# Kernel optimization log

Measured on AMD Instinct MI355X. Metric: run time of the kernel, lower is better.

The kernel has to match this reference:

```python
import jax, jax.numpy as jnp
import numpy as np

D = 256; NH = 8; NL = 4; NP = 4; HD = D // NH
LEVELS = ((80, 80), (40, 40), (20, 20), (10, 10))
B = 8; LTXT = 32
LVIS = sum(h * w for h, w in LEVELS)  # 8500


def layer_norm(x, g, b):
    m = x.mean(-1, keepdims=True)
    v = ((x - m) ** 2).mean(-1, keepdims=True)
    return (x - m) * jax.lax.rsqrt(v + 1e-5) * g + b


def gelu(x):
    return jax.nn.gelu(x, approximate=False)


def sample_level(v, H, W, loc):
    # v: [B,NH,H*W,HD] level value; loc: [B,Lq,NH,NP,2] normalized [0,1] (x,y)
    # bilinear, align_corners=False, zero padding (matches grid_sample in MSDeformAttn)
    x = loc[..., 0] * W - 0.5
    y = loc[..., 1] * H - 0.5
    x0 = jnp.floor(x); y0 = jnp.floor(y)
    fx = x - x0; fy = y - y0
    Bq, Lq = loc.shape[0], loc.shape[1]
    out = jnp.zeros((Bq, NH, Lq * NP, HD), v.dtype)
    for dx in (0, 1):
        for dy in (0, 1):
            xi = x0 + dx; yi = y0 + dy
            w = (fx if dx else 1.0 - fx) * (fy if dy else 1.0 - fy)
            valid = (xi >= 0) & (xi < W) & (yi >= 0) & (yi < H)
            xi_c = jnp.clip(xi, 0, W - 1).astype(jnp.int32)
            yi_c = jnp.clip(yi, 0, H - 1).astype(jnp.int32)
            idx = (yi_c * W + xi_c).transpose(0, 2, 1, 3).reshape(Bq, NH, Lq * NP)
            wv = jnp.where(valid, w, 0.0).transpose(0, 2, 1, 3).reshape(Bq, NH, Lq * NP, 1)
            g = jnp.take_along_axis(v, idx[..., None], axis=2)  # [B,NH,Lq*NP,HD]
            out = out + g * wv
    return out.reshape(Bq, NH, Lq, NP, HD)


def setup_inputs() -> dict:
    key = jax.random.key(0)
    ks = iter(jax.random.split(key, 64))
    def rn(shape, s=1.0):
        return jax.random.normal(next(ks), shape, jnp.float32) * s
    inp = {}
    inp['txt_tokens'] = rn((B, LTXT, D))
    inp['vis_tokens'] = rn((B, LVIS, D))
    for i, (H, W) in enumerate(LEVELS):
        inp[f'feat{i}'] = rn((B, D, H, W))
    inp['spatial_shapes'] = jnp.array(LEVELS, jnp.int32)
    starts = np.cumsum([0] + [h * w for h, w in LEVELS])[:NL]
    inp['level_start_index'] = jnp.array(starts, jnp.int32)
    inp['reference_points'] = jax.random.uniform(next(ks), (B, LTXT, NL, 2), jnp.float32)
    inp['txt_pos'] = rn((B, LTXT, D), 0.02)
    inp['vis_pos'] = rn((B, LVIS, D), 0.02)
    s = 0.02
    # MSDeformAttn params
    inp['W_off'] = rn((D, NH * NL * NP * 2), s); inp['b_off'] = rn((NH * NL * NP * 2,), s)
    inp['W_aw'] = rn((D, NH * NL * NP), s); inp['b_aw'] = rn((NH * NL * NP,), s)
    inp['W_v'] = rn((D, D), s); inp['b_v'] = rn((D,), s)
    inp['W_do'] = rn((D, D), s); inp['b_do'] = rn((D,), s)
    # adapter projections
    inp['W_q_lvi'] = rn((D, D), s); inp['b_q_lvi'] = rn((D,), s)
    inp['W_out_lvi'] = rn((D, D), s); inp['b_out_lvi'] = rn((D,), s)
    # lvi norms + ffn
    inp['ln1_g'] = jnp.ones((D,)); inp['ln1_b'] = jnp.zeros((D,))
    inp['ln2_g'] = jnp.ones((D,)); inp['ln2_b'] = jnp.zeros((D,))
    inp['ffn1_W1'] = rn((D, 4 * D), s); inp['ffn1_b1'] = rn((4 * D,), s)
    inp['ffn1_W2'] = rn((4 * D, D), s); inp['ffn1_b2'] = rn((D,), s)
    # vli MultiheadAttention
    inp['Wq_m'] = rn((D, D), s); inp['bq_m'] = rn((D,), s)
    inp['Wk_m'] = rn((D, D), s); inp['bk_m'] = rn((D,), s)
    inp['Wv_m'] = rn((D, D), s); inp['bv_m'] = rn((D,), s)
    inp['Wo_m'] = rn((D, D), s); inp['bo_m'] = rn((D,), s)
    inp['vln1_g'] = jnp.ones((D,)); inp['vln1_b'] = jnp.zeros((D,))
    inp['vln2_g'] = jnp.ones((D,)); inp['vln2_b'] = jnp.zeros((D,))
    inp['ffn2_W1'] = rn((D, 4 * D), s); inp['ffn2_b1'] = rn((4 * D,), s)
    inp['ffn2_W2'] = rn((4 * D, D), s); inp['ffn2_b2'] = rn((D,), s)
    return inp


def reference(txt_tokens, vis_tokens, feat0, feat1, feat2, feat3, reference_points, txt_pos, vis_pos,
              W_off, b_off, W_aw, b_aw, W_v, b_v, W_do, b_do,
              W_q_lvi, b_q_lvi, W_out_lvi, b_out_lvi,
              ln1_g, ln1_b, ln2_g, ln2_b,
              ffn1_W1, ffn1_b1, ffn1_W2, ffn1_b2,
              Wq_m, bq_m, Wk_m, bk_m, Wv_m, bv_m, Wo_m, bo_m,
              vln1_g, vln1_b, vln2_g, vln2_b,
              ffn2_W1, ffn2_b1, ffn2_W2, ffn2_b2,
              spatial_shapes, level_start_index):
    # ---- lvi: deformable multi-scale attention (txt queries sample vis features) ----
    txt_query = txt_tokens + txt_pos
    q = txt_query @ W_q_lvi + b_q_lvi
    feats = (feat0, feat1, feat2, feat3)
    value = jnp.concatenate([f.reshape(f.shape[0], D, -1).transpose(0, 2, 1) for f in feats], axis=1)
    v = (value @ W_v + b_v).reshape(B, LVIS, NH, HD)
    off = (q @ W_off + b_off).reshape(B, LTXT, NH, NL, NP, 2)
    aw = jax.nn.softmax((q @ W_aw + b_aw).reshape(B, LTXT, NH, NL * NP), axis=-1).reshape(B, LTXT, NH, NL, NP)
    normalizer = jnp.array([[w, h] for h, w in LEVELS], jnp.float32)  # (W,H) per level
    loc = reference_points[:, :, None, :, None, :] + off / normalizer[None, None, None, :, None, :]
    acc = jnp.zeros((B, NH, LTXT, HD), v.dtype)
    start = 0
    for l, (H, W) in enumerate(LEVELS):
        vl = v[:, start:start + H * W].transpose(0, 2, 1, 3)  # [B,NH,HW,HD]
        s = sample_level(vl, H, W, loc[:, :, :, l])           # [B,NH,Lq,NP,HD]
        awl = aw[:, :, :, l].transpose(0, 2, 1, 3)[..., None]  # [B,NH,Lq,NP,1]
        acc = acc + (s * awl).sum(3)
        start += H * W
    d_out = acc.transpose(0, 2, 1, 3).reshape(B, LTXT, D) @ W_do + b_do
    txt_attn = d_out @ W_out_lvi + b_out_lvi
    txt_res = layer_norm(txt_tokens + txt_attn, ln1_g, ln1_b)
    ff = gelu(txt_res @ ffn1_W1 + ffn1_b1) @ ffn1_W2 + ffn1_b2
    txt_res = layer_norm(txt_res + ff, ln2_g, ln2_b)
    # ---- vli: standard cross attention (vis queries attend txt) ----
    vis_query = vis_tokens + vis_pos
    vis_key = txt_res + txt_pos
    qh = (vis_query @ Wq_m + bq_m).reshape(B, LVIS, NH, HD)
    kh = (vis_key @ Wk_m + bk_m).reshape(B, LTXT, NH, HD)
    vh = (vis_key @ Wv_m + bv_m).reshape(B, LTXT, NH, HD)
    scores = jnp.einsum('bqhd,bkhd->bhqk', qh, kh) / np.float32(np.sqrt(HD))
    p = jax.nn.softmax(scores, axis=-1)
    mo = jnp.einsum('bhqk,bkhd->bqhd', p, vh).reshape(B, LVIS, D) @ Wo_m + bo_m
    vis_res = layer_norm(vis_tokens + mo, vln1_g, vln1_b)
    ff2 = gelu(vis_res @ ffn2_W1 + ffn2_b1) @ ffn2_W2 + ffn2_b2
    vis_res = layer_norm(vis_res + ff2, vln2_g, vln2_b)
    attn_weights = p.mean(axis=1)  # torch MHA averages over heads
    return (txt_res, vis_res, attn_weights)
```

## Files before the change

kernel.cpp:

```cpp
#include <hip/hip_runtime.h>
#include <cstddef>

#define DD   256
#define NHH  8
#define HDD  32
#define BB   8
#define LT   32
#define LV   8500

typedef unsigned short u16;
typedef unsigned int   u32;
typedef __attribute__((ext_vector_type(8))) short short8;
typedef __attribute__((ext_vector_type(8))) unsigned short ushort8;
typedef __attribute__((ext_vector_type(4))) float f32x4;

__device__ __forceinline__ float gelu_f(float x) {
  return 0.5f * x * (1.0f + erff(x * 0.70710678118654752440f));
}

__device__ __forceinline__ u16 f2bf(float x) {
  u32 u = __float_as_uint(x);
  u += 0x7FFFu + ((u >> 16) & 1u);
  return (u16)(u >> 16);
}
__device__ __forceinline__ float bf2f(u16 h) { return __uint_as_float((u32)h << 16); }

enum { AM_PLAIN = 0, AM_ADD = 1, AM_FEAT = 2 };
enum { EP_BIAS = 0, EP_GELU = 1, EP_ACC = 2 };

template<int BM, int BN, int TM, int TN, int AMODE, int EPI>
__launch_bounds__(256)
__global__ void gemm_k(const float* __restrict__ A0, const float* __restrict__ A1,
                       const float* __restrict__ Wt, const float* __restrict__ bias,
                       float* __restrict__ C, int M, int K, int ldw, int ldc)
{
  constexpr int BK = 16;
  __shared__ __align__(16) float As[BK][BM];
  __shared__ __align__(16) float Ws[BK][BN];
  const int tid  = threadIdx.x;
  const int row0 = blockIdx.x * BM;
  const int col0 = blockIdx.y * BN;
  const int tx = tid % (BN / TN);
  const int ty = tid / (BN / TN);
  float acc[TM][TN] = {};

  for (int k0 = 0; k0 < K; k0 += BK) {
    {
      constexpr int AU = BM * BK / 4;
      for (int u = tid; u < AU; u += 256) {
        int m  = u / (BK / 4);
        int kq = (u % (BK / 4)) * 4;
        int grow = row0 + m;
        float4 v = make_float4(0.f, 0.f, 0.f, 0.f);
        if (grow < M) {
          v = *(const float4*)(A0 + (size_t)grow * K + k0 + kq);
          if constexpr (AMODE == AM_ADD) {
            float4 w = *(const float4*)(A1 + (size_t)grow * K + k0 + kq);
            v.x += w.x; v.y += w.y; v.z += w.z; v.w += w.w;
          }
        }
        As[kq + 0][m] = v.x; As[kq + 1][m] = v.y;
        As[kq + 2][m] = v.z; As[kq + 3][m] = v.w;
      }
    }
    {
      constexpr int WU = BK * BN / 4;
      for (int u = tid; u < WU; u += 256) {
        int k  = u / (BN / 4);
        int n4 = (u % (BN / 4)) * 4;
        *(float4*)&Ws[k][n4] =
            *(const float4*)(Wt + (size_t)(k0 + k) * ldw + col0 + n4);
      }
    }
    __syncthreads();

    #pragma unroll
    for (int k = 0; k < BK; ++k) {
      float a[TM], bv[TN];
      #pragma unroll
      for (int i = 0; i < TM; ++i) a[i] = As[k][ty * TM + i];
      #pragma unroll
      for (int j = 0; j < TN; j += 4) {
        float4 t4 = *(const float4*)&Ws[k][tx * TN + j];
        bv[j] = t4.x; bv[j + 1] = t4.y; bv[j + 2] = t4.z; bv[j + 3] = t4.w;
      }
      #pragma unroll
      for (int i = 0; i < TM; ++i)
        #pragma unroll
        for (int j = 0; j < TN; ++j)
          acc[i][j] = fmaf(a[i], bv[j], acc[i][j]);
    }
    __syncthreads();
  }

  #pragma unroll
  for (int i = 0; i < TM; ++i) {
    int r = row0 + ty * TM + i;
    if (r >= M) continue;
    #pragma unroll
    for (int j4 = 0; j4 < TN; j4 += 4) {
      int c = col0 + tx * TN + j4;
      float4 v = make_float4(acc[i][j4], acc[i][j4 + 1], acc[i][j4 + 2], acc[i][j4 + 3]);
      float4 b4 = *(const float4*)(bias + c);
      v.x += b4.x; v.y += b4.y; v.z += b4.z; v.w += b4.w;
      if constexpr (EPI == EP_GELU) {
        v.x = gelu_f(v.x); v.y = gelu_f(v.y); v.z = gelu_f(v.z); v.w = gelu_f(v.w);
      }
      *(float4*)(C + (size_t)r * ldc + c) = v;
    }
  }
}

__global__ void wsplit_kernel(const float* __restrict__ W, u16* __restrict__ hi,
                              u16* __restrict__ lo, int total, int Nw)
{
  int id = blockIdx.x * 256 + threadIdx.x;
  if (id >= total) return;
  int k = id / Nw, n = id - k * Nw;
  float x = W[id];
  u16 h = f2bf(x);
  u16 l = f2bf(x - bf2f(h));
  int o = ((k >> 3) * Nw + n) * 8 + (k & 7);
  hi[o] = h; lo[o] = l;
}

template<int AMODE, int EPI>
__global__ __launch_bounds__(256) void mgemm(
    const void* __restrict__ Ap, const float* __restrict__ A1,
    const u16* __restrict__ Whi, const u16* __restrict__ Wlo,
    const float* __restrict__ bias, void* __restrict__ Cp,
    int M, int K, int lda, int ldc, int Nw, int wcol0, int ks0,
    const float* __restrict__ f0, const float* __restrict__ f1,
    const float* __restrict__ f2, const float* __restrict__ f3)
{
  __shared__ __align__(16) u16 Ahi[4 * 129 * 8];
  __shared__ __align__(16) u16 Alo[4 * 129 * 8];
  const int tid  = threadIdx.x;
  const int lane = tid & 63;
  const int w    = tid >> 6;
  const int wr   = w >> 1, wc = w & 1;
  const int row0  = blockIdx.x * 128;
  const int colC0 = blockIdx.y * 128;
  f32x4 acc[4][4] = {};

  const int nk = K >> 5;
  for (int kt = 0; kt < nk; ++kt) {
    if constexpr (AMODE == 3) {
      const u16* Ab = (const u16*)Ap;
      #pragma unroll
      for (int p = 0; p < 2; ++p) {
        int j = tid + p * 256;
        int row = j >> 2, slot = j & 3;
        int gr = row0 + row;
        ushort8 v = {};
        if (gr < M) v = *(const ushort8*)(Ab + (size_t)gr * lda + kt * 32 + slot * 8);
        *(ushort8*)&Ahi[(slot * 129 + row) * 8] = v;
      }
    } else {
      #pragma unroll
      for (int p = 0; p < 4; ++p) {
        int j = tid + p * 256;
        int row, f4;
        if constexpr (AMODE == 2) { f4 = j >> 7; row = j & 127; }
        else                      { row = j >> 3; f4 = j & 7; }
        int gr = row0 + row;
        float4 v = make_float4(0.f, 0.f, 0.f, 0.f);
        if (gr < M) {
          if constexpr (AMODE == 2) {
            int b = gr / LV;
            int s = gr - b * LV;
            int l = (s >= 8400) ? 3 : (s >= 8000) ? 2 : (s >= 6400) ? 1 : 0;
            const float* fp = (l == 0) ? f0 : (l == 1) ? f1 : (l == 2) ? f2 : f3;
            const int hw = (l == 0) ? 6400 : (l == 1) ? 1600 : (l == 2) ? 400 : 100;
            const int st = (l == 0) ? 0 : (l == 1) ? 6400 : (l == 2) ? 8000 : 8400;
            const float* base = fp + ((size_t)b * DD + (kt * 32 + f4 * 4)) * hw + (s - st);
            v.x = base[0];
            v.y = base[(size_t)hw];
            v.z = base[2 * (size_t)hw];
            v.w = base[3 * (size_t)hw];
          } else {
            const float* Af = (const float*)Ap;
            v = *(const float4*)(Af + (size_t)gr * lda + kt * 32 + f4 * 4);
            if constexpr (AMODE == 1) {
              float4 u2 = *(const float4*)(A1 + (size_t)gr * lda + kt * 32 + f4 * 4);
              v.x += u2.x; v.y += u2.y; v.z += u2.z; v.w += u2.w;
            }
          }
        }
        int slot = f4 >> 1, half = f4 & 1;
        int off = (slot * 129 + row) * 8 + half * 4;
        u16 h0 = f2bf(v.x), h1 = f2bf(v.y), h2 = f2bf(v.z), h3 = f2bf(v.w);
        uint2 hp; hp.x = (u32)h0 | ((u32)h1 << 16); hp.y = (u32)h2 | ((u32)h3 << 16);
        *(uint2*)&Ahi[off] = hp;
        u16 l0 = f2bf(v.x - bf2f(h0)), l1 = f2bf(v.y - bf2f(h1));
        u16 l2 = f2bf(v.z - bf2f(h2)), l3 = f2bf(v.w - bf2f(h3));
        uint2 lp; lp.x = (u32)l0 | ((u32)l1 << 16); lp.y = (u32)l2 | ((u32)l3 << 16);
        *(uint2*)&Alo[off] = lp;
      }
    }
    __syncthreads();

    const int slot = lane >> 4;
    const int lrow = lane & 15;
    short8 ah[4], al[4], bh[4], bl[4];
    #pragma unroll
    for (int m = 0; m < 4; ++m) {
      int off = (slot * 129 + wr * 64 + m * 16 + lrow) * 8;
      ah[m] = *(const short8*)&Ahi[off];
      if constexpr (AMODE != 3) al[m] = *(const short8*)&Alo[off];
    }
    #pragma unroll
    for (int n = 0; n < 4; ++n) {
      size_t off = ((size_t)((ks0 + kt) * 4 + slot) * Nw + wcol0 + colC0 + wc * 64 + n * 16 + lrow) * 8;
      bh[n] = *(const short8*)(Whi + off);
      bl[n] = *(const short8*)(Wlo + off);
    }
    #pragma unroll
    for (int m = 0; m < 4; ++m)
      #pragma unroll
      for (int n = 0; n < 4; ++n) {
        acc[m][n] = __builtin_amdgcn_mfma_f32_16x16x32_bf16(ah[m], bh[n], acc[m][n], 0, 0, 0);
        acc[m][n] = __builtin_amdgcn_mfma_f32_16x16x32_bf16(ah[m], bl[n], acc[m][n], 0, 0, 0);
        if constexpr (AMODE != 3)
          acc[m][n] = __builtin_amdgcn_mfma_f32_16x16x32_bf16(al[m], bh[n], acc[m][n], 0, 0, 0);
      }
    __syncthreads();
  }

  const int lrow = lane & 15;
  #pragma unroll
  for (int m = 0; m < 4; ++m) {
    #pragma unroll
    for (int j = 0; j < 4; ++j) {
      int r = row0 + wr * 64 + m * 16 + ((lane >> 4) << 2) + j;
      if (r >= M) continue;
      #pragma unroll
      for (int n = 0; n < 4; ++n) {
        int c = colC0 + wc * 64 + n * 16 + lrow;
        float v = acc[m][n][j];
        if constexpr (EPI == 0) {
          ((float*)Cp)[(size_t)r * ldc + c] = v + bias[c];
        } else if constexpr (EPI == 1) {
          ((u16*)Cp)[(size_t)r * ldc + c] = f2bf(gelu_f(v + bias[c]));
        } else {
          ((float*)Cp)[(size_t)r * ldc + c] += v;
        }
      }
    }
  }
}

__global__ void ln_kernel(const float* __restrict__ X, const float* __restrict__ R,
                          const float* __restrict__ g, const float* __restrict__ bta,
                          float* __restrict__ O, int M)
{
  int row  = blockIdx.x * 4 + (threadIdx.x >> 6);
  int lane = threadIdx.x & 63;
  if (row >= M) return;
  size_t base = (size_t)row * DD + lane * 4;
  float4 x = *(const float4*)(X + base);
  float4 r = *(const float4*)(R + base);
  x.x += r.x; x.y += r.y; x.z += r.z; x.w += r.w;
  float s  = x.x + x.y + x.z + x.w;
  float s2 = x.x * x.x + x.y * x.y + x.z * x.z + x.w * x.w;
  #pragma unroll
  for (int m = 1; m < 64; m <<= 1) {
    s  += __shfl_xor(s, m);
    s2 += __shfl_xor(s2, m);
  }
  float mean = s * (1.0f / 256.0f);
  float var  = s2 * (1.0f / 256.0f) - mean * mean;
  float rstd = rsqrtf(var + 1e-5f);
  float4 gg = *(const float4*)(g + lane * 4);
  float4 bb = *(const float4*)(bta + lane * 4);
  float4 o;
  o.x = (x.x - mean) * rstd * gg.x + bb.x;
  o.y = (x.y - mean) * rstd * gg.y + bb.y;
  o.z = (x.z - mean) * rstd * gg.z + bb.z;
  o.w = (x.w - mean) * rstd * gg.w + bb.w;
  *(float4*)(O + base) = o;
}

__global__ void softloc_kernel(const float* __restrict__ awl, const float* __restrict__ offb,
                               const float* __restrict__ refp, float* __restrict__ aw,
                               float* __restrict__ loc)
{
  int idx = blockIdx.x * 256 + threadIdx.x;
  if (idx >= BB * LT * NHH) return;
  int h   = idx & 7;
  int row = idx >> 3;
  float v[16]; float mx = -1e30f;
  #pragma unroll
  for (int i = 0; i < 16; ++i) { v[i] = awl[row * 128 + h * 16 + i]; mx = fmaxf(mx, v[i]); }
  float sum = 0.f;
  #pragma unroll
  for (int i = 0; i < 16; ++i) { v[i] = expf(v[i] - mx); sum += v[i]; }
  float inv = 1.0f / sum;
  #pragma unroll
  for (int i = 0; i < 16; ++i) aw[row * 128 + h * 16 + i] = v[i] * inv;
  const float invn[4] = {1.f / 80.f, 1.f / 40.f, 1.f / 20.f, 1.f / 10.f};
  #pragma unroll
  for (int l = 0; l < 4; ++l) {
    float rx = refp[(row * 4 + l) * 2 + 0];
    float ry = refp[(row * 4 + l) * 2 + 1];
    #pragma unroll
    for (int p = 0; p < 4; ++p) {
      int o = row * 256 + h * 32 + l * 8 + p * 2;
      loc[o + 0] = rx + offb[o + 0] * invn[l];
      loc[o + 1] = ry + offb[o + 1] * invn[l];
    }
  }
}

__global__ void sampler_kernel(const float* __restrict__ vproj, const float* __restrict__ loc,
                               const float* __restrict__ aw, float* __restrict__ acc)
{
  int row = blockIdx.x;
  int t   = threadIdx.x;
  int h   = t >> 5, hd = t & 31;
  int b   = row >> 5;
  const float* vb = vproj + (size_t)b * LV * DD;
  const int Hs[4] = {80, 40, 20, 10};
  const int st[4] = {0, 6400, 8000, 8400};
  float a = 0.f;
  #pragma unroll
  for (int l = 0; l < 4; ++l) {
    const int Wl = Hs[l], Hl = Hs[l];
    #pragma unroll
    for (int p = 0; p < 4; ++p) {
      int o = row * 256 + h * 32 + l * 8 + p * 2;
      float lx  = loc[o + 0];
      float ly  = loc[o + 1];
      float wgt = aw[row * 128 + h * 16 + l * 4 + p];
      float x = lx * (float)Wl - 0.5f;
      float y = ly * (float)Hl - 0.5f;
      float x0f = floorf(x), y0f = floorf(y);
      float fx = x - x0f, fy = y - y0f;
      int x0 = (int)x0f, y0 = (int)y0f;
      #pragma unroll
      for (int dy = 0; dy < 2; ++dy) {
        #pragma unroll
        for (int dx = 0; dx < 2; ++dx) {
          int xi = x0 + dx, yi = y0 + dy;
          float w2 = (dx ? fx : 1.f - fx) * (dy ? fy : 1.f - fy);
          if (xi >= 0 && xi < Wl && yi >= 0 && yi < Hl) {
            a = fmaf(wgt * w2, vb[(size_t)(st[l] + yi * Wl + xi) * DD + h * 32 + hd], a);
          }
        }
      }
    }
  }
  acc[(size_t)row * DD + t] = a;
}

__global__ __launch_bounds__(512)
void attn_kernel(const float* __restrict__ qh, const float* __restrict__ kh,
                 const float* __restrict__ vh, float* __restrict__ mo,
                 float* __restrict__ awout)
{
  __shared__ __align__(16) float Ks[32][256];
  __shared__ __align__(16) float Vs[32][256];
  const int b = blockIdx.y;
  {
    const float4* ksrc = (const float4*)(kh + (size_t)b * 32 * DD);
    const float4* vsrc = (const float4*)(vh + (size_t)b * 32 * DD);
    float4* kd = (float4*)&Ks[0][0];
    float4* vd = (float4*)&Vs[0][0];
    for (int u = threadIdx.x; u < 2048; u += 512) { kd[u] = ksrc[u]; vd[u] = vsrc[u]; }
  }
  __syncthreads();

  const int rl   = threadIdx.x >> 5;
  const int l    = threadIdx.x & 31;
  const int h    = l >> 2;
  const int part = l & 3;
  const int s    = blockIdx.x * 16 + rl;
  if (s >= LV) return;
  const size_t row = (size_t)b * LV + s;
  const int c0 = h * 32 + part * 8;
  const float scale = 0.17677669529663687f;

  float q[8];
  {
    const float4* qp = (const float4*)(qh + row * DD + c0);
    float4 a = qp[0], c = qp[1];
    q[0]=a.x; q[1]=a.y; q[2]=a.z; q[3]=a.w; q[4]=c.x; q[5]=c.y; q[6]=c.z; q[7]=c.w;
  }

  float sc[32]; float mx = -1e30f;
  #pragma unroll
  for (int k = 0; k < 32; ++k) {
    const float4* kp = (const float4*)&Ks[k][c0];
    float4 a = kp[0], c = kp[1];
    float d = 0.f;
    d = fmaf(q[0], a.x, d); d = fmaf(q[1], a.y, d); d = fmaf(q[2], a.z, d); d = fmaf(q[3], a.w, d);
    d = fmaf(q[4], c.x, d); d = fmaf(q[5], c.y, d); d = fmaf(q[6], c.z, d); d = fmaf(q[7], c.w, d);
    d += __shfl_xor(d, 1);
    d += __shfl_xor(d, 2);
    sc[k] = d * scale;
    mx = fmaxf(mx, sc[k]);
  }
  float sum = 0.f;
  #pragma unroll
  for (int k = 0; k < 32; ++k) { sc[k] = expf(sc[k] - mx); sum += sc[k]; }
  const float inv = 1.0f / sum;
  #pragma unroll
  for (int k = 0; k < 32; ++k) sc[k] *= inv;

  float o[8] = {};
  #pragma unroll
  for (int k = 0; k < 32; ++k) {
    const float4* vp = (const float4*)&Vs[k][c0];
    float4 a = vp[0], c = vp[1];
    const float pk = sc[k];
    o[0] = fmaf(pk, a.x, o[0]); o[1] = fmaf(pk, a.y, o[1]);
    o[2] = fmaf(pk, a.z, o[2]); o[3] = fmaf(pk, a.w, o[3]);
    o[4] = fmaf(pk, c.x, o[4]); o[5] = fmaf(pk, c.y, o[5]);
    o[6] = fmaf(pk, c.z, o[6]); o[7] = fmaf(pk, c.w, o[7]);
  }
  {
    float4* op = (float4*)(mo + row * DD + c0);
    op[0] = make_float4(o[0], o[1], o[2], o[3]);
    op[1] = make_float4(o[4], o[5], o[6], o[7]);
  }
  #pragma unroll
  for (int k = 0; k < 32; ++k) {
    float v = sc[k];
    v += __shfl_xor(v, 4);
    v += __shfl_xor(v, 8);
    v += __shfl_xor(v, 16);
    if (h == 0 && (k >> 3) == part) awout[row * 32 + k] = v * 0.125f;
  }
}

extern "C" void kernel_launch(void* const* d_in, const int* in_sizes, int n_in,
                              void* d_out, int out_size, void* d_ws, size_t ws_size,
                              hipStream_t stream)
{
  const float* txt_tokens = (const float*)d_in[0];
  const float* vis_tokens = (const float*)d_in[1];
  const float* feat0 = (const float*)d_in[2];
  const float* feat1 = (const float*)d_in[3];
  const float* feat2 = (const float*)d_in[4];
  const float* feat3 = (const float*)d_in[5];
  const float* refp    = (const float*)d_in[8];
  const float* txt_pos = (const float*)d_in[9];
  const float* vis_pos = (const float*)d_in[10];
  const float* W_off = (const float*)d_in[11]; const float* b_off = (const float*)d_in[12];
  const float* W_aw  = (const float*)d_in[13]; const float* b_aw  = (const float*)d_in[14];
  const float* W_v   = (const float*)d_in[15]; const float* b_v   = (const float*)d_in[16];
  const float* W_do  = (const float*)d_in[17]; const float* b_do  = (const float*)d_in[18];
  const float* W_q   = (const float*)d_in[19]; const float* b_q   = (const float*)d_in[20];
  const float* W_out = (const float*)d_in[21]; const float* b_out = (const float*)d_in[22];
  const float* ln1_g = (const float*)d_in[23]; const float* ln1_b = (const float*)d_in[24];
  const float* ln2_g = (const float*)d_in[25]; const float* ln2_b = (const float*)d_in[26];
  const float* f1W1  = (const float*)d_in[27]; const float* f1b1  = (const float*)d_in[28];
  const float* f1W2  = (const float*)d_in[29]; const float* f1b2  = (const float*)d_in[30];
  const float* Wq_m  = (const float*)d_in[31]; const float* bq_m  = (const float*)d_in[32];
  const float* Wk_m  = (const float*)d_in[33]; const float* bk_m  = (const float*)d_in[34];
  const float* Wv_m  = (const float*)d_in[35]; const float* bv_m  = (const float*)d_in[36];
  const float* Wo_m  = (const float*)d_in[37]; const float* bo_m  = (const float*)d_in[38];
  const float* vln1_g = (const float*)d_in[39]; const float* vln1_b = (const float*)d_in[40];
  const float* vln2_g = (const float*)d_in[41]; const float* vln2_b = (const float*)d_in[42];
  const float* f2W1  = (const float*)d_in[43]; const float* f2b1  = (const float*)d_in[44];
  const float* f2W2  = (const float*)d_in[45]; const float* f2b2  = (const float*)d_in[46];

  const int MV = BB * LV;
  float* ws = (float*)d_ws;
  const size_t BIG = (size_t)MV * DD;
  float* buf0 = ws;
  float* buf1 = ws + BIG;
  float* buf2 = ws + 2 * BIG;
  float* sm   = ws + 3 * BIG;
  float* qb    = sm;
  float* offb  = qb + 65536;
  float* awlb  = offb + 65536;
  float* awb   = awlb + 32768;
  float* locb  = awb + 32768;
  float* accb  = locb + 65536;
  float* doutb = accb + 65536;
  float* tattn = doutb + 65536;
  float* tres1 = tattn + 65536;
  float* ffh   = tres1 + 65536;
  float* ffb   = ffh + 262144;
  float* khb   = ffb + 65536;
  float* vhb   = khb + 65536;
  u16* wsp   = (u16*)(vhb + 65536);
  u16* wv_hi = wsp;               u16* wv_lo = wv_hi + 65536;
  u16* wq_hi = wv_lo + 65536;     u16* wq_lo = wq_hi + 65536;
  u16* wo_hi = wq_lo + 65536;     u16* wo_lo = wo_hi + 65536;
  u16* w1_hi = wo_lo + 65536;     u16* w1_lo = w1_hi + 262144;
  u16* w2_hi = w1_lo + 262144;    u16* w2_lo = w2_hi + 262144;

  float* out_txt = (float*)d_out;
  float* out_vis = out_txt + (size_t)BB * LT * DD;
  float* out_aw  = out_vis + BIG;

  dim3 blk(256);
  #define NOF nullptr, nullptr, nullptr, nullptr

  wsplit_kernel<<<256, blk, 0, stream>>>(W_v,  wv_hi, wv_lo, 65536, 256);
  wsplit_kernel<<<256, blk, 0, stream>>>(Wq_m, wq_hi, wq_lo, 65536, 256);
  wsplit_kernel<<<256, blk, 0, stream>>>(Wo_m, wo_hi, wo_lo, 65536, 256);
  wsplit_kernel<<<1024, blk, 0, stream>>>(f2W1, w1_hi, w1_lo, 262144, 1024);
  wsplit_kernel<<<1024, blk, 0, stream>>>(f2W2, w2_hi, w2_lo, 262144, 256);

  mgemm<2, 0><<<dim3(532, 2), blk, 0, stream>>>(
      nullptr, nullptr, wv_hi, wv_lo, b_v, buf0, MV, DD, DD, DD, DD, 0, 0,
      feat0, feat1, feat2, feat3);
  mgemm<1, 0><<<dim3(532, 2), blk, 0, stream>>>(
      vis_tokens, vis_pos, wq_hi, wq_lo, bq_m, buf1, MV, DD, DD, DD, DD, 0, 0, NOF);

  gemm_k<32,64,2,4,AM_ADD,EP_BIAS><<<dim3(8,4), blk, 0, stream>>>(
      txt_tokens, txt_pos, W_q, b_q, qb, 256, DD, DD, DD);
  gemm_k<32,64,2,4,AM_PLAIN,EP_BIAS><<<dim3(8,4), blk, 0, stream>>>(
      qb, nullptr, W_off, b_off, offb, 256, DD, DD, DD);
  gemm_k<32,64,2,4,AM_PLAIN,EP_BIAS><<<dim3(8,2), blk, 0, stream>>>(
      qb, nullptr, W_aw, b_aw, awlb, 256, DD, 128, 128);
  softloc_kernel<<<8, blk, 0, stream>>>(awlb, offb, refp, awb, locb);
  sampler_kernel<<<256, blk, 0, stream>>>(buf0, locb, awb, accb);
  gemm_k<32,64,2,4,AM_PLAIN,EP_BIAS><<<dim3(8,4), blk, 0, stream>>>(
      accb, nullptr, W_do, b_do, doutb, 256, DD, DD, DD);
  gemm_k<32,64,2,4,AM_PLAIN,EP_BIAS><<<dim3(8,4), blk, 0, stream>>>(
      doutb, nullptr, W_out, b_out, tattn, 256, DD, DD, DD);
  ln_kernel<<<64, blk, 0, stream>>>(tattn, txt_tokens, ln1_g, ln1_b, tres1, 256);
  gemm_k<32,64,2,4,AM_PLAIN,EP_GELU><<<dim3(8,16), blk, 0, stream>>>(
      tres1, nullptr, f1W1, f1b1, ffh, 256, DD, 1024, 1024);
  gemm_k<32,64,2,4,AM_PLAIN,EP_BIAS><<<dim3(8,4), blk, 0, stream>>>(
      ffh, nullptr, f1W2, f1b2, ffb, 256, 1024, DD, DD);
  ln_kernel<<<64, blk, 0, stream>>>(ffb, tres1, ln2_g, ln2_b, out_txt, 256);

  gemm_k<32,64,2,4,AM_ADD,EP_BIAS><<<dim3(8,4), blk, 0, stream>>>(
      out_txt, txt_pos, Wk_m, bk_m, khb, 256, DD, DD, DD);
  gemm_k<32,64,2,4,AM_ADD,EP_BIAS><<<dim3(8,4), blk, 0, stream>>>(
      out_txt, txt_pos, Wv_m, bv_m, vhb, 256, DD, DD, DD);

  attn_kernel<<<dim3(532, 8), dim3(512), 0, stream>>>(buf1, khb, vhb, buf2, out_aw);
  mgemm<0, 0><<<dim3(532, 2), blk, 0, stream>>>(
      buf2, nullptr, wo_hi, wo_lo, bo_m, buf0, MV, DD, DD, DD, DD, 0, 0, NOF);
  ln_kernel<<<17000, blk, 0, stream>>>(buf0, vis_tokens, vln1_g, vln1_b, buf1, MV);

  for (int c = 0; c < 2; ++c) {
    mgemm<0, 1><<<dim3(532, 4), blk, 0, stream>>>(
        buf1, nullptr, w1_hi, w1_lo, f2b1 + c * 512, buf2,
        MV, DD, DD, 512, 1024, c * 512, 0, NOF);
    if (c == 0) {
      mgemm<3, 0><<<dim3(532, 2), blk, 0, stream>>>(
          buf2, nullptr, w2_hi, w2_lo, f2b2, buf0,
          MV, 512, 512, DD, DD, 0, 0, NOF);
    } else {
      mgemm<3, 2><<<dim3(532, 2), blk, 0, stream>>>(
          buf2, nullptr, w2_hi, w2_lo, nullptr, buf0,
          MV, 512, 512, DD, DD, 0, 16, NOF);
    }
  }
  ln_kernel<<<17000, blk, 0, stream>>>(buf0, buf1, vln2_g, vln2_b, out_vis, MV);
  #undef NOF
}
```

Baseline: 1.302 ms.

## Pre-split activations to bf16 hi/lo and double-buffer A tiles via global_load_lds

The attention kernel and the first vision LayerNorm now write their outputs already split into bf16 hi/lo pairs. The matching GEMMs can then stream A tiles straight into LDS with global_load_lds, double-buffered, instead of converting fp32 in registers on every tile. The attention kernel also stops staging K/V in shared memory and reads them from global/cache directly. The second LayerNorm rebuilds the residual from the hi/lo pair, which changes the intermediate precision slightly. Overall this trades extra activation write traffic for removing per-tile conversion work and overlapping loads with MFMA.

```diff
diff --git a/kernel.cpp b/kernel.cpp
--- a/kernel.cpp
+++ b/kernel.cpp
@@ -25,7 +25,13 @@
 }
 __device__ __forceinline__ float bf2f(u16 h) { return __uint_as_float((u32)h << 16); }
 
-enum { AM_PLAIN = 0, AM_ADD = 1, AM_FEAT = 2 };
+__device__ __forceinline__ void gload16(const u16* g, u16* l) {
+  __builtin_amdgcn_global_load_lds(
+      (const __attribute__((address_space(1))) void*)g,
+      (__attribute__((address_space(3))) void*)l, 16, 0, 0);
+}
+
+enum { AM_PLAIN = 0, AM_ADD = 1, AM_FEAT = 2, AM_HI = 3, AM_SPLIT = 4 };
 enum { EP_BIAS = 0, EP_GELU = 1, EP_ACC = 2 };
 
 template<int BM, int BN, int TM, int TN, int AMODE, int EPI>
@@ -126,15 +132,16 @@
 
 template<int AMODE, int EPI>
 __global__ __launch_bounds__(256) void mgemm(
-    const void* __restrict__ Ap, const float* __restrict__ A1,
+    const void* __restrict__ Ap, const void* __restrict__ A1p,
     const u16* __restrict__ Whi, const u16* __restrict__ Wlo,
     const float* __restrict__ bias, void* __restrict__ Cp,
     int M, int K, int lda, int ldc, int Nw, int wcol0, int ks0,
     const float* __restrict__ f0, const float* __restrict__ f1,
     const float* __restrict__ f2, const float* __restrict__ f3)
 {
-  __shared__ __align__(16) u16 Ahi[4 * 129 * 8];
-  __shared__ __align__(16) u16 Alo[4 * 129 * 8];
+  constexpr bool GL = (AMODE >= 3);
+  constexpr int SMEM_U16 = GL ? (AMODE == AM_SPLIT ? 16384 : 8192) : 8256;
+  __shared__ __align__(16) u16 smem[SMEM_U16];
   const int tid  = threadIdx.x;
   const int lane = tid & 63;
   const int w    = tid >> 6;
@@ -142,31 +149,68 @@
   const int row0  = blockIdx.x * 128;
   const int colC0 = blockIdx.y * 128;
   f32x4 acc[4][4] = {};
-
   const int nk = K >> 5;
-  for (int kt = 0; kt < nk; ++kt) {
-    if constexpr (AMODE == 3) {
-      const u16* Ab = (const u16*)Ap;
+
+  if constexpr (GL) {
+    const u16* Ah = (const u16*)Ap;
+    const u16* Al = (const u16*)A1p;
+    auto stage = [&](int t, int buf) {
       #pragma unroll
       for (int p = 0; p < 2; ++p) {
-        int j = tid + p * 256;
-        int row = j >> 2, slot = j & 3;
-        int gr = row0 + row;
-        ushort8 v = {};
-        if (gr < M) v = *(const ushort8*)(Ab + (size_t)gr * lda + kt * 32 + slot * 8);
-        *(ushort8*)&Ahi[(slot * 129 + row) * 8] = v;
-      }
-    } else {
+        int i = w + p * 4;
+        int r = row0 + i * 16 + (lane >> 2);
+        if (r >= M) r = M - 1;
+        size_t goff = (size_t)r * lda + t * 32 + (lane & 3) * 8;
+        gload16(Ah + goff, &smem[buf * 4096 + i * 512]);
+        if constexpr (AMODE == AM_SPLIT)
+          gload16(Al + goff, &smem[8192 + buf * 4096 + i * 512]);
+      }
+    };
+    stage(0, 0);
+    __syncthreads();
+    for (int kt = 0; kt < nk; ++kt) {
+      const int cur = kt & 1;
+      if (kt + 1 < nk) stage(kt + 1, cur ^ 1);
+      const int slot = lane >> 4;
+      const int lrow = lane & 15;
+      short8 ah[4], al[4], bh[4], bl[4];
+      #pragma unroll
+      for (int m = 0; m < 4; ++m) {
+        int off = cur * 4096 + (((wr * 64 + m * 16 + lrow) << 2) + slot) * 8;
+        ah[m] = *(const short8*)&smem[off];
+        if constexpr (AMODE == AM_SPLIT) al[m] = *(const short8*)&smem[8192 + off];
+      }
+      #pragma unroll
+      for (int n = 0; n < 4; ++n) {
+        size_t off = ((size_t)((ks0 + kt) * 4 + slot) * Nw + wcol0 + colC0 + wc * 64 + n * 16 + lrow) * 8;
+        bh[n] = *(const short8*)(Whi + off);
+        bl[n] = *(const short8*)(Wlo + off);
+      }
+      #pragma unroll
+      for (int m = 0; m < 4; ++m)
+        #pragma unroll
+        for (int n = 0; n < 4; ++n) {
+          acc[m][n] = __builtin_amdgcn_mfma_f32_16x16x32_bf16(ah[m], bh[n], acc[m][n], 0, 0, 0);
+          acc[m][n] = __builtin_amdgcn_mfma_f32_16x16x32_bf16(ah[m], bl[n], acc[m][n], 0, 0, 0);
+          if constexpr (AMODE == AM_SPLIT)
+            acc[m][n] = __builtin_amdgcn_mfma_f32_16x16x32_bf16(al[m], bh[n], acc[m][n], 0, 0, 0);
+        }
+      __syncthreads();
+    }
+  } else {
+    u16* Ahi = smem;
+    u16* Alo = smem + 4128;
+    for (int kt = 0; kt < nk; ++kt) {
       #pragma unroll
       for (int p = 0; p < 4; ++p) {
         int j = tid + p * 256;
         int row, f4;
-        if constexpr (AMODE == 2) { f4 = j >> 7; row = j & 127; }
-        else                      { row = j >> 3; f4 = j & 7; }
+        if constexpr (AMODE == AM_FEAT) { f4 = j >> 7; row = j & 127; }
+        else                            { row = j >> 3; f4 = j & 7; }
         int gr = row0 + row;
         float4 v = make_float4(0.f, 0.f, 0.f, 0.f);
         if (gr < M) {
-          if constexpr (AMODE == 2) {
+          if constexpr (AMODE == AM_FEAT) {
             int b = gr / LV;
             int s = gr - b * LV;
             int l = (s >= 8400) ? 3 : (s >= 8000) ? 2 : (s >= 6400) ? 1 : 0;
@@ -181,8 +225,8 @@
           } else {
             const float* Af = (const float*)Ap;
             v = *(const float4*)(Af + (size_t)gr * lda + kt * 32 + f4 * 4);
-            if constexpr (AMODE == 1) {
-              float4 u2 = *(const float4*)(A1 + (size_t)gr * lda + kt * 32 + f4 * 4);
+            if constexpr (AMODE == AM_ADD) {
+              float4 u2 = *(const float4*)((const float*)A1p + (size_t)gr * lda + kt * 32 + f4 * 4);
               v.x += u2.x; v.y += u2.y; v.z += u2.z; v.w += u2.w;
             }
           }
@@ -197,34 +241,33 @@
         uint2 lp; lp.x = (u32)l0 | ((u32)l1 << 16); lp.y = (u32)l2 | ((u32)l3 << 16);
         *(uint2*)&Alo[off] = lp;
       }
-    }
-    __syncthreads();
-
-    const int slot = lane >> 4;
-    const int lrow = lane & 15;
-    short8 ah[4], al[4], bh[4], bl[4];
-    #pragma unroll
-    for (int m = 0; m < 4; ++m) {
-      int off = (slot * 129 + wr * 64 + m * 16 + lrow) * 8;
-      ah[m] = *(const short8*)&Ahi[off];
-      if constexpr (AMODE != 3) al[m] = *(const short8*)&Alo[off];
-    }
-    #pragma unroll
-    for (int n = 0; n < 4; ++n) {
-      size_t off = ((size_t)((ks0 + kt) * 4 + slot) * Nw + wcol0 + colC0 + wc * 64 + n * 16 + lrow) * 8;
-      bh[n] = *(const short8*)(Whi + off);
-      bl[n] = *(const short8*)(Wlo + off);
-    }
-    #pragma unroll
-    for (int m = 0; m < 4; ++m)
+      __syncthreads();
+
+      const int slot = lane >> 4;
+      const int lrow = lane & 15;
+      short8 ah[4], al[4], bh[4], bl[4];
+      #pragma unroll
+      for (int m = 0; m < 4; ++m) {
+        int off = (slot * 129 + wr * 64 + m * 16 + lrow) * 8;
+        ah[m] = *(const short8*)&Ahi[off];
+        al[m] = *(const short8*)&Alo[off];
+      }
       #pragma unroll
       for (int n = 0; n < 4; ++n) {
-        acc[m][n] = __builtin_amdgcn_mfma_f32_16x16x32_bf16(ah[m], bh[n], acc[m][n], 0, 0, 0);
-        acc[m][n] = __builtin_amdgcn_mfma_f32_16x16x32_bf16(ah[m], bl[n], acc[m][n], 0, 0, 0);
-        if constexpr (AMODE != 3)
+        size_t off = ((size_t)((ks0 + kt) * 4 + slot) * Nw + wcol0 + colC0 + wc * 64 + n * 16 + lrow) * 8;
+        bh[n] = *(const short8*)(Whi + off);
+        bl[n] = *(const short8*)(Wlo + off);
+      }
+      #pragma unroll
+      for (int m = 0; m < 4; ++m)
+        #pragma unroll
+        for (int n = 0; n < 4; ++n) {
+          acc[m][n] = __builtin_amdgcn_mfma_f32_16x16x32_bf16(ah[m], bh[n], acc[m][n], 0, 0, 0);
+          acc[m][n] = __builtin_amdgcn_mfma_f32_16x16x32_bf16(ah[m], bl[n], acc[m][n], 0, 0, 0);
           acc[m][n] = __builtin_amdgcn_mfma_f32_16x16x32_bf16(al[m], bh[n], acc[m][n], 0, 0, 0);
-      }
-    __syncthreads();
+        }
+      __syncthreads();
+    }
   }
 
   const int lrow = lane & 15;
@@ -238,9 +281,9 @@
       for (int n = 0; n < 4; ++n) {
         int c = colC0 + wc * 64 + n * 16 + lrow;
         float v = acc[m][n][j];
-        if constexpr (EPI == 0) {
+        if constexpr (EPI == EP_BIAS) {
           ((float*)Cp)[(size_t)r * ldc + c] = v + bias[c];
-        } else if constexpr (EPI == 1) {
+        } else if constexpr (EPI == EP_GELU) {
           ((u16*)Cp)[(size_t)r * ldc + c] = f2bf(gelu_f(v + bias[c]));
         } else {
           ((float*)Cp)[(size_t)r * ldc + c] += v;
@@ -250,17 +293,7 @@
   }
 }
 
-__global__ void ln_kernel(const float* __restrict__ X, const float* __restrict__ R,
-                          const float* __restrict__ g, const float* __restrict__ bta,
-                          float* __restrict__ O, int M)
-{
-  int row  = blockIdx.x * 4 + (threadIdx.x >> 6);
-  int lane = threadIdx.x & 63;
-  if (row >= M) return;
-  size_t base = (size_t)row * DD + lane * 4;
-  float4 x = *(const float4*)(X + base);
-  float4 r = *(const float4*)(R + base);
-  x.x += r.x; x.y += r.y; x.z += r.z; x.w += r.w;
+__device__ __forceinline__ float4 ln_core(float4 x, const float* g, const float* bta, int lane) {
   float s  = x.x + x.y + x.z + x.w;
   float s2 = x.x * x.x + x.y * x.y + x.z * x.z + x.w * x.w;
   #pragma unroll
@@ -278,6 +311,61 @@
   o.y = (x.y - mean) * rstd * gg.y + bb.y;
   o.z = (x.z - mean) * rstd * gg.z + bb.z;
   o.w = (x.w - mean) * rstd * gg.w + bb.w;
+  return o;
+}
+
+__global__ void ln_kernel(const float* __restrict__ X, const float* __restrict__ R,
+                          const float* __restrict__ g, const float* __restrict__ bta,
+                          float* __restrict__ O, int M)
+{
+  int row  = blockIdx.x * 4 + (threadIdx.x >> 6);
+  int lane = threadIdx.x & 63;
+  if (row >= M) return;
+  size_t base = (size_t)row * DD + lane * 4;
+  float4 x = *(const float4*)(X + base);
+  float4 r = *(const float4*)(R + base);
+  x.x += r.x; x.y += r.y; x.z += r.z; x.w += r.w;
+  float4 o = ln_core(x, g, bta, lane);
+  *(float4*)(O + base) = o;
+}
+
+__global__ void ln_vis1(const float* __restrict__ X, const float* __restrict__ R,
+                        const float* __restrict__ g, const float* __restrict__ bta,
+                        u16* __restrict__ Oh, u16* __restrict__ Ol, int M)
+{
+  int row  = blockIdx.x * 4 + (threadIdx.x >> 6);
+  int lane = threadIdx.x & 63;
+  if (row >= M) return;
+  size_t base = (size_t)row * DD + lane * 4;
+  float4 x = *(const float4*)(X + base);
+  float4 r = *(const float4*)(R + base);
+  x.x += r.x; x.y += r.y; x.z += r.z; x.w += r.w;
+  float4 o = ln_core(x, g, bta, lane);
+  u16 h0 = f2bf(o.x), h1 = f2bf(o.y), h2 = f2bf(o.z), h3 = f2bf(o.w);
+  uint2 hp; hp.x = (u32)h0 | ((u32)h1 << 16); hp.y = (u32)h2 | ((u32)h3 << 16);
+  *(uint2*)(Oh + base) = hp;
+  u16 l0 = f2bf(o.x - bf2f(h0)), l1 = f2bf(o.y - bf2f(h1));
+  u16 l2 = f2bf(o.z - bf2f(h2)), l3 = f2bf(o.w - bf2f(h3));
+  uint2 lp; lp.x = (u32)l0 | ((u32)l1 << 16); lp.y = (u32)l2 | ((u32)l3 << 16);
+  *(uint2*)(Ol + base) = lp;
+}
+
+__global__ void ln_vis2(const float* __restrict__ X, const u16* __restrict__ Rh,
+                        const u16* __restrict__ Rl, const float* __restrict__ g,
+                        const float* __restrict__ bta, float* __restrict__ O, int M)
+{
+  int row  = blockIdx.x * 4 + (threadIdx.x >> 6);
+  int lane = threadIdx.x & 63;
+  if (row >= M) return;
+  size_t base = (size_t)row * DD + lane * 4;
+  float4 x = *(const float4*)(X + base);
+  uint2 hp = *(const uint2*)(Rh + base);
+  uint2 lp = *(const uint2*)(Rl + base);
+  x.x += bf2f((u16)hp.x) + bf2f((u16)lp.x);
+  x.y += bf2f((u16)(hp.x >> 16)) + bf2f((u16)(lp.x >> 16));
+  x.z += bf2f((u16)hp.y) + bf2f((u16)lp.y);
+  x.w += bf2f((u16)(hp.y >> 16)) + bf2f((u16)(lp.y >> 16));
+  float4 o = ln_core(x, g, bta, lane);
   *(float4*)(O + base) = o;
 }
 
@@ -355,30 +443,21 @@
 
 __global__ __launch_bounds__(512)
 void attn_kernel(const float* __restrict__ qh, const float* __restrict__ kh,
-                 const float* __restrict__ vh, float* __restrict__ mo,
-                 float* __restrict__ awout)
-{
-  __shared__ __align__(16) float Ks[32][256];
-  __shared__ __align__(16) float Vs[32][256];
-  const int b = blockIdx.y;
-  {
-    const float4* ksrc = (const float4*)(kh + (size_t)b * 32 * DD);
-    const float4* vsrc = (const float4*)(vh + (size_t)b * 32 * DD);
-    float4* kd = (float4*)&Ks[0][0];
-    float4* vd = (float4*)&Vs[0][0];
-    for (int u = threadIdx.x; u < 2048; u += 512) { kd[u] = ksrc[u]; vd[u] = vsrc[u]; }
-  }
-  __syncthreads();
-
-  const int rl   = threadIdx.x >> 5;
-  const int l    = threadIdx.x & 31;
-  const int h    = l >> 2;
+                 const float* __restrict__ vh, u16* __restrict__ mo_hi,
+                 u16* __restrict__ mo_lo, float* __restrict__ awout)
+{
+  const int b  = blockIdx.y;
+  const int rl = threadIdx.x >> 5;
+  const int l  = threadIdx.x & 31;
+  const int h  = l >> 2;
   const int part = l & 3;
-  const int s    = blockIdx.x * 16 + rl;
+  const int s  = blockIdx.x * 16 + rl;
   if (s >= LV) return;
   const size_t row = (size_t)b * LV + s;
   const int c0 = h * 32 + part * 8;
   const float scale = 0.17677669529663687f;
+  const float* Kb = kh + (size_t)b * 32 * DD;
+  const float* Vb = vh + (size_t)b * 32 * DD;
 
   float q[8];
   {
@@ -390,7 +469,7 @@
   float sc[32]; float mx = -1e30f;
   #pragma unroll
   for (int k = 0; k < 32; ++k) {
-    const float4* kp = (const float4*)&Ks[k][c0];
+    const float4* kp = (const float4*)(Kb + k * DD + c0);
     float4 a = kp[0], c = kp[1];
     float d = 0.f;
     d = fmaf(q[0], a.x, d); d = fmaf(q[1], a.y, d); d = fmaf(q[2], a.z, d); d = fmaf(q[3], a.w, d);
@@ -410,7 +489,7 @@
   float o[8] = {};
   #pragma unroll
   for (int k = 0; k < 32; ++k) {
-    const float4* vp = (const float4*)&Vs[k][c0];
+    const float4* vp = (const float4*)(Vb + k * DD + c0);
     float4 a = vp[0], c = vp[1];
     const float pk = sc[k];
     o[0] = fmaf(pk, a.x, o[0]); o[1] = fmaf(pk, a.y, o[1]);
@@ -419,9 +498,19 @@
     o[6] = fmaf(pk, c.z, o[6]); o[7] = fmaf(pk, c.w, o[7]);
   }
   {
-    float4* op = (float4*)(mo + row * DD + c0);
-    op[0] = make_float4(o[0], o[1], o[2], o[3]);
-    op[1] = make_float4(o[4], o[5], o[6], o[7]);
+    u16 hh[8], ll[8];
+    #pragma unroll
+    for (int j = 0; j < 8; ++j) {
+      hh[j] = f2bf(o[j]);
+      ll[j] = f2bf(o[j] - bf2f(hh[j]));
+    }
+    uint4 hp, lp;
+    hp.x = (u32)hh[0] | ((u32)hh[1] << 16); hp.y = (u32)hh[2] | ((u32)hh[3] << 16);
+    hp.z = (u32)hh[4] | ((u32)hh[5] << 16); hp.w = (u32)hh[6] | ((u32)hh[7] << 16);
+    lp.x = (u32)ll[0] | ((u32)ll[1] << 16); lp.y = (u32)ll[2] | ((u32)ll[3] << 16);
+    lp.z = (u32)ll[4] | ((u32)ll[5] << 16); lp.w = (u32)ll[6] | ((u32)ll[7] << 16);
+    *(uint4*)(mo_hi + row * DD + c0) = hp;
+    *(uint4*)(mo_lo + row * DD + c0) = lp;
   }
   #pragma unroll
   for (int k = 0; k < 32; ++k) {
@@ -492,6 +581,10 @@
   u16* w1_hi = wo_lo + 65536;     u16* w1_lo = w1_hi + 262144;
   u16* w2_hi = w1_lo + 262144;    u16* w2_lo = w2_hi + 262144;
 
+  u16* mo_hi = (u16*)buf2;  u16* mo_lo = mo_hi + BIG;
+  u16* ln_hi = (u16*)buf1;  u16* ln_lo = ln_hi + BIG;
+  u16* hid   = (u16*)buf2;
+
   float* out_txt = (float*)d_out;
   float* out_vis = out_txt + (size_t)BB * LT * DD;
   float* out_aw  = out_vis + BIG;
@@ -505,10 +598,10 @@
   wsplit_kernel<<<1024, blk, 0, stream>>>(f2W1, w1_hi, w1_lo, 262144, 1024);
   wsplit_kernel<<<1024, blk, 0, stream>>>(f2W2, w2_hi, w2_lo, 262144, 256);
 
-  mgemm<2, 0><<<dim3(532, 2), blk, 0, stream>>>(
+  mgemm<AM_FEAT, EP_BIAS><<<dim3(532, 2), blk, 0, stream>>>(
       nullptr, nullptr, wv_hi, wv_lo, b_v, buf0, MV, DD, DD, DD, DD, 0, 0,
       feat0, feat1, feat2, feat3);
-  mgemm<1, 0><<<dim3(532, 2), blk, 0, stream>>>(
+  mgemm<AM_ADD, EP_BIAS><<<dim3(532, 2), blk, 0, stream>>>(
       vis_tokens, vis_pos, wq_hi, wq_lo, bq_m, buf1, MV, DD, DD, DD, DD, 0, 0, NOF);
 
   gemm_k<32,64,2,4,AM_ADD,EP_BIAS><<<dim3(8,4), blk, 0, stream>>>(
@@ -535,25 +628,25 @@
   gemm_k<32,64,2,4,AM_ADD,EP_BIAS><<<dim3(8,4), blk, 0, stream>>>(
       out_txt, txt_pos, Wv_m, bv_m, vhb, 256, DD, DD, DD);
 
-  attn_kernel<<<dim3(532, 8), dim3(512), 0, stream>>>(buf1, khb, vhb, buf2, out_aw);
-  mgemm<0, 0><<<dim3(532, 2), blk, 0, stream>>>(
-      buf2, nullptr, wo_hi, wo_lo, bo_m, buf0, MV, DD, DD, DD, DD, 0, 0, NOF);
-  ln_kernel<<<17000, blk, 0, stream>>>(buf0, vis_tokens, vln1_g, vln1_b, buf1, MV);
+  attn_kernel<<<dim3(532, 8), dim3(512), 0, stream>>>(buf1, khb, vhb, mo_hi, mo_lo, out_aw);
+  mgemm<AM_SPLIT, EP_BIAS><<<dim3(532, 2), blk, 0, stream>>>(
+      mo_hi, mo_lo, wo_hi, wo_lo, bo_m, buf0, MV, DD, 256, DD, DD, 0, 0, NOF);
+  ln_vis1<<<17000, blk, 0, stream>>>(buf0, vis_tokens, vln1_g, vln1_b, ln_hi, ln_lo, MV);
 
   for (int c = 0; c < 2; ++c) {
-    mgemm<0, 1><<<dim3(532, 4), blk, 0, stream>>>(
-        buf1, nullptr, w1_hi, w1_lo, f2b1 + c * 512, buf2,
-        MV, DD, DD, 512, 1024, c * 512, 0, NOF);
+    mgemm<AM_SPLIT, EP_GELU><<<dim3(532, 4), blk, 0, stream>>>(
+        ln_hi, ln_lo, w1_hi, w1_lo, f2b1 + c * 512, hid,
+        MV, DD, 256, 512, 1024, c * 512, 0, NOF);
     if (c == 0) {
-      mgemm<3, 0><<<dim3(532, 2), blk, 0, stream>>>(
-          buf2, nullptr, w2_hi, w2_lo, f2b2, buf0,
+      mgemm<AM_HI, EP_BIAS><<<dim3(532, 2), blk, 0, stream>>>(
+          hid, nullptr, w2_hi, w2_lo, f2b2, buf0,
           MV, 512, 512, DD, DD, 0, 0, NOF);
     } else {
-      mgemm<3, 2><<<dim3(532, 2), blk, 0, stream>>>(
-          buf2, nullptr, w2_hi, w2_lo, nullptr, buf0,
+      mgemm<AM_HI, EP_ACC><<<dim3(532, 2), blk, 0, stream>>>(
+          hid, nullptr, w2_hi, w2_lo, nullptr, buf0,
           MV, 512, 512, DD, DD, 0, 16, NOF);
     }
   }
-  ln_kernel<<<17000, blk, 0, stream>>>(buf0, buf1, vln2_g, vln2_b, out_vis, MV);
+  ln_vis2<<<17000, blk, 0, stream>>>(buf0, ln_hi, ln_lo, vln2_g, vln2_b, out_vis, MV);
   #undef NOF
 }
```

After: 1.288 ms. No clear change (-1.1%).
